# Performance work log

Hardware: AMD Instinct MI355X
Metric: run time of the kernel (lower is better)

The kernel has to match this reference:

```python
import jax, jax.numpy as jnp
import numpy as np

N_NODES = 50000
N_EDGES = 400000
D = 64          # in_feats == out_feats (transform=False)
DIST_DIM = 32
NUM = 5         # num_neighbor
N_BOUND = 64    # embedding table rows = N_BOUND + 1


def setup_inputs() -> dict:
    key = jax.random.key(0)
    ks = jax.random.split(key, 9)
    feat = jax.random.normal(ks[0], (N_NODES, D), dtype=jnp.float32)
    loc = jax.random.uniform(ks[1], (N_NODES, 2), dtype=jnp.float32)
    embed_table = jax.random.normal(ks[2], (N_BOUND + 1, DIST_DIM), dtype=jnp.float32)
    G_w = jax.random.normal(ks[3], (D, DIST_DIM), dtype=jnp.float32) / np.sqrt(DIST_DIM)
    agg_w = jax.random.normal(ks[4], (D, 2 * D), dtype=jnp.float32) / np.sqrt(2 * D)
    agg_b = jnp.zeros((D,), dtype=jnp.float32)
    boundaries = jnp.linspace(0.0, 2.0, N_BOUND).astype(jnp.float32)
    src = jax.random.randint(ks[5], (N_EDGES,), 0, N_NODES, dtype=jnp.int32)
    dst = jax.random.randint(ks[6], (N_EDGES,), 0, N_NODES, dtype=jnp.int32)
    inter_ids = jax.random.randint(ks[7], (N_EDGES, NUM), 0, N_NODES, dtype=jnp.int32)
    return {"feat": feat, "loc": loc, "embed_table": embed_table, "G_w": G_w,
            "agg_w": agg_w, "agg_b": agg_b, "boundaries": boundaries,
            "src": src, "dst": dst, "inter_ids": inter_ids}


def reference(feat, loc, embed_table, G_w, agg_w, agg_b, boundaries, src, dst, inter_ids):
    n = feat.shape[0]
    e, num = inter_ids.shape
    one = jnp.ones((e,), dtype=jnp.float32)
    # degrees: d0 = in_deg^-0.5 (at dst), d2 = out_deg^-0.5 (at src), clamp(min=1)
    in_deg = jnp.maximum(jax.ops.segment_sum(one, dst, num_segments=n), 1.0)
    out_deg = jnp.maximum(jax.ops.segment_sum(one, src, num_segments=n), 1.0)
    d0 = in_deg ** -0.5  # [N]
    d2 = out_deg ** -0.5  # [N]
    # dist1: dst->src node distance per edge
    loc_src = loc[src]                                   # [E,2]
    dist1 = jnp.linalg.norm(loc[dst] - loc_src, axis=1)  # [E]
    # dist_: src to each sampled intermediate node
    inter_pos = loc[inter_ids]                                     # [E,num,2]
    dist_ = jnp.linalg.norm(loc_src[:, None, :] - inter_pos, axis=-1)  # [E,num]
    # bucketize (torch right=False == searchsorted side='left') -> embed -> linear G
    b1 = jnp.searchsorted(boundaries, dist1, side='left')   # [E]
    b_ = jnp.searchsorted(boundaries, dist_, side='left')   # [E,num]
    dist_embed1 = embed_table[b1] @ G_w.T                    # [E,D]
    dist_embed_ = embed_table[b_] @ G_w.T                    # [E,num,D]
    # mean over sampled intermediates of (dist-embed * gathered feat)
    dist_embed_dot_h = (dist_embed_ * feat[inter_ids]).mean(axis=1)  # [E,D]
    # agg_fc on concat, degree-scaled
    cat = jnp.concatenate([dist_embed1 * feat[src], dist_embed_dot_h], axis=1)  # [E,2D]
    h = (d0[dst] * d2[src])[:, None] * (cat @ agg_w.T + agg_b)                  # [E,D]
    # copy_e / sum: scatter-sum edges to dst nodes
    rst = jax.ops.segment_sum(h, dst, num_segments=n)  # [N,D]
    return rst
```

## Files before the change

kernel.cpp:

```cpp
#include <hip/hip_runtime.h>


#define DFEAT 64

typedef __attribute__((ext_vector_type(8))) _Float16 half8;
typedef __attribute__((ext_vector_type(4))) float floatx4;
typedef __attribute__((ext_vector_type(4))) int intx4;

__device__ __forceinline__ void sb8d(int2 q, float (&f)[8]) {
#pragma unroll
    for (int t = 0; t < 4; ++t) f[t] = (float)((q.x << (24 - 8 * t)) >> 24);
#pragma unroll
    for (int t = 0; t < 4; ++t) f[4 + t] = (float)((q.y << (24 - 8 * t)) >> 24);
}

__device__ __forceinline__ int bucketize(float x, float bnd) {
    int i = (int)(x * 31.5f);
    i = min(max(i, 0), 64);
#pragma unroll
    for (int t = 0; t < 3; ++t) {
        float bi = __shfl(bnd, min(i, 63));
        if (i < 64 && bi < x) ++i;
    }
#pragma unroll
    for (int t = 0; t < 2; ++t) {
        float bim = __shfl(bnd, max(i - 1, 0));
        if (i > 0 && bim >= x) --i;
    }
    return i;
}

__global__ void k_prep(const float* __restrict__ Etab,
                       const float* __restrict__ G, float* __restrict__ P,
                       float* __restrict__ rst, float* __restrict__ degs,
                       const float* __restrict__ feat,
                       signed char* __restrict__ featQ,
                       float* __restrict__ scaleQ, int nRst, int nDeg) {
    int i = blockIdx.x * blockDim.x + threadIdx.x;
    if (i < nDeg) degs[i] = 0.0f;
    if (i < 65 * DFEAT) {
        int b = i >> 6, o = i & 63;
        float a = 0.0f;
#pragma unroll
        for (int m = 0; m < 32; ++m)
            a = fmaf(Etab[b * 32 + m], G[o * 32 + m], a);
        P[i] = a;
    }
    if (i < nRst) {
        __builtin_nontemporal_store(0.0f, rst + i);
        if (featQ) {
            float f = feat[i];
            float a = fabsf(f);
#pragma unroll
            for (int o = 32; o; o >>= 1) a = fmaxf(a, __shfl_xor(a, o));
            float inv = (a > 0.0f) ? 127.0f / a : 0.0f;
            __builtin_nontemporal_store(
                (signed char)__float2int_rn(f * inv), featQ + i);
            if ((i & 63) == 0) scaleQ[i >> 6] = a * (1.0f / 127.0f);
        }
    }
}

__global__ void k_deg(const int* __restrict__ src, const int* __restrict__ dst,
                      float* __restrict__ degs, int N, int E) {
    int i = blockIdx.x * blockDim.x + threadIdx.x;
    if (i < E) {
        atomicAdd(&degs[dst[i]], 1.0f);
        atomicAdd(&degs[N + src[i]], 1.0f);
    }
}

#define SCHUNK 1024

__global__ void k_scanA(const float* __restrict__ degs, int* __restrict__ bsum,
                        int N) {
    __shared__ int part[256];
    const int t = threadIdx.x;
    const int base = blockIdx.x * SCHUNK + t * 4;
    int s = 0;
#pragma unroll
    for (int j = 0; j < 4; ++j) {
        int i = base + j;
        if (i < N) s += (int)degs[i];
    }
    part[t] = s;
    __syncthreads();
    for (int off = 128; off; off >>= 1) {
        if (t < off) part[t] += part[t + off];
        __syncthreads();
    }
    if (t == 0) bsum[blockIdx.x] = part[0];
}

__global__ void k_scanB(int* __restrict__ bsum, int NB) {
    if (threadIdx.x == 0) {
        int run = 0;
        for (int i = 0; i < NB; ++i) {
            int v = bsum[i];
            bsum[i] = run;
            run += v;
        }
    }
}

__global__ void k_scanC(const float* __restrict__ degs,
                        const int* __restrict__ bsum, int* __restrict__ binptr,
                        int N) {
    __shared__ int part[256];
    const int t = threadIdx.x;
    const int base = blockIdx.x * SCHUNK + t * 4;
    int c[4];
    int s = 0;
#pragma unroll
    for (int j = 0; j < 4; ++j) {
        int i = base + j;
        c[j] = (i < N) ? (int)degs[i] : 0;
        s += c[j];
    }
    part[t] = s;
    __syncthreads();
    for (int off = 1; off < 256; off <<= 1) {
        int v = (t >= off) ? part[t - off] : 0;
        __syncthreads();
        part[t] += v;
        __syncthreads();
    }
    int run = bsum[blockIdx.x] + part[t] - s;
#pragma unroll
    for (int j = 0; j < 4; ++j) {
        int i = base + j;
        if (i < N) {
            binptr[i] = run;
            run += c[j];
        }
    }
}

__global__ void k_scatter(const int* __restrict__ src,
                          const int* __restrict__ dst,
                          const int* __restrict__ inter,
                          int* __restrict__ binptr, int* __restrict__ pack,
                          int E, int paddedE) {
    int i = blockIdx.x * blockDim.x + threadIdx.x;
    if (i < E) {
        int dd = dst[i];
        int pos = atomicAdd(&binptr[dd], 1);
        intx4 p0 = {src[i], dd, inter[i * 5 + 0], inter[i * 5 + 1]};
        intx4 p1 = {inter[i * 5 + 2], inter[i * 5 + 3], inter[i * 5 + 4], 0};
        __builtin_nontemporal_store(p0, (intx4*)(pack + (size_t)pos * 8));
        __builtin_nontemporal_store(p1, (intx4*)(pack + (size_t)pos * 8 + 4));
    } else if (i < paddedE) {
        intx4 z = {0, 0, 0, 0};
        __builtin_nontemporal_store(z, (intx4*)(pack + (size_t)i * 8));
        __builtin_nontemporal_store(z, (intx4*)(pack + (size_t)i * 8 + 4));
    }
}

#define PPAD 68

__global__ __launch_bounds__(256, 4) void k_edge(
    const float* __restrict__ feat, const signed char* __restrict__ featQ,
    const float* __restrict__ scaleQ, const float* __restrict__ loc,
    const float* __restrict__ agg_w, const float* __restrict__ agg_b,
    const float* __restrict__ bnds, const int* __restrict__ src,
    const int* __restrict__ dst, const int* __restrict__ inter,
    const int* __restrict__ pack, const float* __restrict__ P,
    const float* __restrict__ degs, float* __restrict__ rst, int N, int E) {
    const int tid = threadIdx.x;
    const int lane = tid & 63;
    const int wid = tid >> 6;
    const int m16 = lane & 15;
    const int quad = lane >> 4;

    __shared__ float sP[65 * PPAD];
    __shared__ half8 sWB[16 * 64];

    for (int i = tid; i < 65 * DFEAT; i += 256)
        sP[(i >> 6) * PPAD + (i & 63)] = P[i];

    for (int f = wid; f < 16; f += 4) {
        int sl = f >> 2, nt = f & 3;
        const float* wp = agg_w + (nt * 16 + m16) * 128 + sl * 32 + quad * 8;
        floatx4 wa = *(const floatx4*)wp;
        floatx4 wb = *(const floatx4*)(wp + 4);
        float xs[8] = {wa.x, wa.y, wa.z, wa.w, wb.x, wb.y, wb.z, wb.w};
        half8 h;
#pragma unroll
        for (int j = 0; j < 8; ++j) h[j] = (_Float16)xs[j];
        sWB[f * 64 + lane] = h;
    }

    const float bnd = bnds[lane];
    float bias4[4];
#pragma unroll
    for (int nt = 0; nt < 4; ++nt) bias4[nt] = agg_b[nt * 16 + m16];

    __syncthreads();

    const int nw = gridDim.x << 2;
    const int wi = (blockIdx.x << 2) + wid;
    const int ngroups = (E + 15) >> 4;
    const bool haveQ = (featQ != nullptr);
    const int k0q = quad * 8;

    const int qq = ngroups / nw, rr = ngroups - qq * nw;
    const int g0 = wi * qq + min(wi, rr);
    const int g1 = g0 + qq + (wi < rr ? 1 : 0);

    for (int g = g0; g < g1; ++g) {
        const int em = (g << 4) + m16;
        const bool act = em < E;
        const int ec = act ? em : 0;

        int s, d, ij[5];
        if (pack) {
            const intx4 p0 = __builtin_nontemporal_load(
                (const intx4*)(pack + (size_t)em * 8));
            const intx4 p1 = __builtin_nontemporal_load(
                (const intx4*)(pack + (size_t)em * 8 + 4));
            s = p0[0]; d = p0[1];
            ij[0] = p0[2]; ij[1] = p0[3];
            ij[2] = p1[0]; ij[3] = p1[1]; ij[4] = p1[2];
        } else {
            s = __builtin_nontemporal_load(src + ec);
            d = __builtin_nontemporal_load(dst + ec);
#pragma unroll
            for (int j = 0; j < 5; ++j)
                ij[j] = __builtin_nontemporal_load(inter + ec * 5 + j);
        }

        const float2 ls = ((const float2*)loc)[s];
        const float2 ld = ((const float2*)loc)[d];
        float2 lj[5];
#pragma unroll
        for (int j = 0; j < 5; ++j) lj[j] = ((const float2*)loc)[ij[j]];
        const float dgd = degs[d];
        const float dgs = degs[N + s];

        half8 A[4];
        float dsc;
        int b1;
        if (haveQ) {
            const float ssrc = scaleQ[s];
            float sq[5];
#pragma unroll
            for (int j = 0; j < 5; ++j) sq[j] = scaleQ[ij[j]];

            const signed char* qrow = featQ + (s << 6);
            int2 qu[2];
            qu[0] = *(const int2*)(qrow + k0q);
            qu[1] = *(const int2*)(qrow + 32 + k0q);
            int2 qv[2][5];
#pragma unroll
            for (int sl = 0; sl < 2; ++sl)
#pragma unroll
                for (int j = 0; j < 5; ++j)
                    qv[sl][j] =
                        *(const int2*)(featQ + (ij[j] << 6) + sl * 32 + k0q);

            dsc = rsqrtf(fmaxf(dgd, 1.0f)) * rsqrtf(fmaxf(dgs, 1.0f));
            if (!act) dsc = 0.0f;
            float dx = ld.x - ls.x, dy = ld.y - ls.y;
            b1 = bucketize(sqrtf(dx * dx + dy * dy), bnd);
            int bj[5];
#pragma unroll
            for (int j = 0; j < 5; ++j) {
                float ex = ls.x - lj[j].x, ey = ls.y - lj[j].y;
                bj[j] = bucketize(sqrtf(ex * ex + ey * ey), bnd);
            }

            const float* prow = sP + b1 * PPAD;
#pragma unroll
            for (int sl = 0; sl < 2; ++sl) {
                int k0 = sl * 32 + k0q;
                float fq[8];
                sb8d(qu[sl], fq);
                floatx4 pa = *(const floatx4*)(prow + k0);
                floatx4 pb = *(const floatx4*)(prow + k0 + 4);
                float xs[8] = {fq[0] * ssrc * pa.x, fq[1] * ssrc * pa.y,
                               fq[2] * ssrc * pa.z, fq[3] * ssrc * pa.w,
                               fq[4] * ssrc * pb.x, fq[5] * ssrc * pb.y,
                               fq[6] * ssrc * pb.z, fq[7] * ssrc * pb.w};
                half8 h;
#pragma unroll
                for (int j = 0; j < 8; ++j) h[j] = (_Float16)xs[j];
                A[sl] = h;
            }
#pragma unroll
            for (int sl = 0; sl < 2; ++sl) {
                int k0 = sl * 32 + k0q;
                float r[8] = {0, 0, 0, 0, 0, 0, 0, 0};
#pragma unroll
                for (int j = 0; j < 5; ++j) {
                    float fq[8];
                    sb8d(qv[sl][j], fq);
                    const float sj = sq[j];
                    const float* pr = sP + bj[j] * PPAD;
                    floatx4 pa = *(const floatx4*)(pr + k0);
                    floatx4 pb = *(const floatx4*)(pr + k0 + 4);
                    r[0] = fmaf(fq[0] * sj, pa.x, r[0]);
                    r[1] = fmaf(fq[1] * sj, pa.y, r[1]);
                    r[2] = fmaf(fq[2] * sj, pa.z, r[2]);
                    r[3] = fmaf(fq[3] * sj, pa.w, r[3]);
                    r[4] = fmaf(fq[4] * sj, pb.x, r[4]);
                    r[5] = fmaf(fq[5] * sj, pb.y, r[5]);
                    r[6] = fmaf(fq[6] * sj, pb.z, r[6]);
                    r[7] = fmaf(fq[7] * sj, pb.w, r[7]);
                }
                half8 h;
#pragma unroll
                for (int j = 0; j < 8; ++j) h[j] = (_Float16)(r[j] * 0.2f);
                A[2 + sl] = h;
            }
        } else {
            dsc = rsqrtf(fmaxf(dgd, 1.0f)) * rsqrtf(fmaxf(dgs, 1.0f));
            if (!act) dsc = 0.0f;
            float dx = ld.x - ls.x, dy = ld.y - ls.y;
            b1 = bucketize(sqrtf(dx * dx + dy * dy), bnd);
            int bj[5];
#pragma unroll
            for (int j = 0; j < 5; ++j) {
                float ex = ls.x - lj[j].x, ey = ls.y - lj[j].y;
                bj[j] = bucketize(sqrtf(ex * ex + ey * ey), bnd);
            }
            const float* frow = feat + (s << 6);
            const float* prow = sP + b1 * PPAD;
#pragma unroll
            for (int sl = 0; sl < 2; ++sl) {
                int k0 = sl * 32 + k0q;
                floatx4 fa = *(const floatx4*)(frow + k0);
                floatx4 fb = *(const floatx4*)(frow + k0 + 4);
                floatx4 pa = *(const floatx4*)(prow + k0);
                floatx4 pb = *(const floatx4*)(prow + k0 + 4);
                float xs[8] = {fa.x * pa.x, fa.y * pa.y, fa.z * pa.z,
                               fa.w * pa.w, fb.x * pb.x, fb.y * pb.y,
                               fb.z * pb.z, fb.w * pb.w};
                half8 h;
#pragma unroll
                for (int j = 0; j < 8; ++j) h[j] = (_Float16)xs[j];
                A[sl] = h;
            }
#pragma unroll
            for (int sl = 0; sl < 2; ++sl) {
                int k0 = sl * 32 + k0q;
                float r[8] = {0, 0, 0, 0, 0, 0, 0, 0};
#pragma unroll
                for (int j = 0; j < 5; ++j) {
                    const float* fr = feat + (ij[j] << 6);
                    const float* pr = sP + bj[j] * PPAD;
                    floatx4 fa = *(const floatx4*)(fr + k0);
                    floatx4 fb = *(const floatx4*)(fr + k0 + 4);
                    floatx4 pa = *(const floatx4*)(pr + k0);
                    floatx4 pb = *(const floatx4*)(pr + k0 + 4);
                    r[0] = fmaf(fa.x, pa.x, r[0]);
                    r[1] = fmaf(fa.y, pa.y, r[1]);
                    r[2] = fmaf(fa.z, pa.z, r[2]);
                    r[3] = fmaf(fa.w, pa.w, r[3]);
                    r[4] = fmaf(fb.x, pb.x, r[4]);
                    r[5] = fmaf(fb.y, pb.y, r[5]);
                    r[6] = fmaf(fb.z, pb.z, r[6]);
                    r[7] = fmaf(fb.w, pb.w, r[7]);
                }
                half8 h;
#pragma unroll
                for (int j = 0; j < 8; ++j) h[j] = (_Float16)(r[j] * 0.2f);
                A[2 + sl] = h;
            }
        }

        floatx4 acc[4] = {{0, 0, 0, 0}, {0, 0, 0, 0}, {0, 0, 0, 0}, {0, 0, 0, 0}};
#pragma unroll
        for (int sl = 0; sl < 4; ++sl) {
#pragma unroll
            for (int nt = 0; nt < 4; ++nt) {
                half8 b = sWB[((sl << 2) + nt) * 64 + lane];
                acc[nt] = __builtin_amdgcn_mfma_f32_16x16x32_f16(
                    A[sl], b, acc[nt], 0, 0, 0);
            }
        }

        const int q4 = quad << 2;
        const int dm0 = __shfl(d, q4 + 0), dm1 = __shfl(d, q4 + 1);
        const int dm2 = __shfl(d, q4 + 2), dm3 = __shfl(d, q4 + 3);
        const float sc0 = __shfl(dsc, q4 + 0), sc1 = __shfl(dsc, q4 + 1);
        const float sc2 = __shfl(dsc, q4 + 2), sc3 = __shfl(dsc, q4 + 3);
        const int dmn = __shfl(d, (q4 + 4) & 15);
        const int dmp = __shfl(d, (q4 - 1) & 15);
        const bool eq0 = dm0 == dm1, eq1 = dm1 == dm2, eq2 = dm2 == dm3;
        const bool eq3 = (quad < 3) && (dm3 == dmn);
        const bool lnk = (quad > 0) && (dmp == dm0);
        const bool alls = eq0 && eq1 && eq2;
        const bool gate = alls && lnk;

        float w0[4], w1[4], w2[4], w3[4], Ci[4];
#pragma unroll
        for (int nt = 0; nt < 4; ++nt) {
            w0[nt] = (acc[nt][0] + bias4[nt]) * sc0;
            w1[nt] = (acc[nt][1] + bias4[nt]) * sc1;
            w2[nt] = (acc[nt][2] + bias4[nt]) * sc2;
            w3[nt] = (acc[nt][3] + bias4[nt]) * sc3;
            if (eq0) w1[nt] += w0[nt];
            if (eq1) w2[nt] += w1[nt];
            if (eq2) w3[nt] += w2[nt];
            float T = w3[nt];
#pragma unroll
            for (int k = 0; k < 3; ++k) {
                float Tp = __shfl(T, (lane - 16) & 63);
                T = w3[nt] + (gate ? Tp : 0.0f);
            }
            float c = __shfl(T, (lane - 16) & 63);
            Ci[nt] = lnk ? c : 0.0f;
        }

        if (!eq0) {
            float* ap = rst + (dm0 << 6) + m16;
            float v0 = w0[0] + Ci[0], v1 = w0[1] + Ci[1];
            float v2 = w0[2] + Ci[2], v3 = w0[3] + Ci[3];
            asm volatile("global_atomic_add_f32 %0, %1, off nt" :: "v"(ap), "v"(v0));
            asm volatile("global_atomic_add_f32 %0, %1, off offset:64 nt" :: "v"(ap), "v"(v1));
            asm volatile("global_atomic_add_f32 %0, %1, off offset:128 nt" :: "v"(ap), "v"(v2));
            asm volatile("global_atomic_add_f32 %0, %1, off offset:192 nt" :: "v"(ap), "v"(v3));
        }
        if (!eq1) {
            float* ap = rst + (dm1 << 6) + m16;
            float h0 = eq0 ? Ci[0] : 0.0f, h1 = eq0 ? Ci[1] : 0.0f;
            float h2 = eq0 ? Ci[2] : 0.0f, h3 = eq0 ? Ci[3] : 0.0f;
            float v0 = w1[0] + h0, v1 = w1[1] + h1;
            float v2 = w1[2] + h2, v3 = w1[3] + h3;
            asm volatile("global_atomic_add_f32 %0, %1, off nt" :: "v"(ap), "v"(v0));
            asm volatile("global_atomic_add_f32 %0, %1, off offset:64 nt" :: "v"(ap), "v"(v1));
            asm volatile("global_atomic_add_f32 %0, %1, off offset:128 nt" :: "v"(ap), "v"(v2));
            asm volatile("global_atomic_add_f32 %0, %1, off offset:192 nt" :: "v"(ap), "v"(v3));
        }
        if (!eq2) {
            const bool hr = eq0 && eq1;
            float* ap = rst + (dm2 << 6) + m16;
            float v0 = w2[0] + (hr ? Ci[0] : 0.0f), v1 = w2[1] + (hr ? Ci[1] : 0.0f);
            float v2 = w2[2] + (hr ? Ci[2] : 0.0f), v3 = w2[3] + (hr ? Ci[3] : 0.0f);
            asm volatile("global_atomic_add_f32 %0, %1, off nt" :: "v"(ap), "v"(v0));
            asm volatile("global_atomic_add_f32 %0, %1, off offset:64 nt" :: "v"(ap), "v"(v1));
            asm volatile("global_atomic_add_f32 %0, %1, off offset:128 nt" :: "v"(ap), "v"(v2));
            asm volatile("global_atomic_add_f32 %0, %1, off offset:192 nt" :: "v"(ap), "v"(v3));
        }
        if (!eq3) {
            float* ap = rst + (dm3 << 6) + m16;
            float v0 = w3[0] + (alls ? Ci[0] : 0.0f), v1 = w3[1] + (alls ? Ci[1] : 0.0f);
            float v2 = w3[2] + (alls ? Ci[2] : 0.0f), v3 = w3[3] + (alls ? Ci[3] : 0.0f);
            asm volatile("global_atomic_add_f32 %0, %1, off nt" :: "v"(ap), "v"(v0));
            asm volatile("global_atomic_add_f32 %0, %1, off offset:64 nt" :: "v"(ap), "v"(v1));
            asm volatile("global_atomic_add_f32 %0, %1, off offset:128 nt" :: "v"(ap), "v"(v2));
            asm volatile("global_atomic_add_f32 %0, %1, off offset:192 nt" :: "v"(ap), "v"(v3));
        }
    }
}

extern "C" void kernel_launch(void* const* d_in, const int* in_sizes, int n_in,
                              void* d_out, int out_size, void* d_ws,
                              size_t ws_size, hipStream_t stream) {
    const float* feat  = (const float*)d_in[0];
    const float* loc   = (const float*)d_in[1];
    const float* embed = (const float*)d_in[2];
    const float* G_w   = (const float*)d_in[3];
    const float* agg_w = (const float*)d_in[4];
    const float* agg_b = (const float*)d_in[5];
    const float* bnds  = (const float*)d_in[6];
    const int* src   = (const int*)d_in[7];
    const int* dst   = (const int*)d_in[8];
    const int* inter = (const int*)d_in[9];

    const int N = in_sizes[0] / DFEAT;
    const int E = in_sizes[7];
    const int ngroups = (E + 15) >> 4;
    const int paddedE = ngroups << 4;
    const int NB = (N + SCHUNK - 1) / SCHUNK;

    float* rst = (float*)d_out;
    float* ws = (float*)d_ws;
    float* degs = ws;
    float* P = ws + 2 * (size_t)N;
    float* scaleQ = P + 65 * DFEAT;

    size_t fixed_bytes = (2 * (size_t)N + 65 * DFEAT + (size_t)N) * sizeof(float);
    size_t fq_off = (fixed_bytes + 15) & ~(size_t)15;
    size_t need_q = fq_off + (size_t)N * DFEAT;
    signed char* featQ =
        (ws_size >= need_q) ? (signed char*)((char*)d_ws + fq_off) : nullptr;

    size_t so = (need_q + 15) & ~(size_t)15;
    size_t need_sort =
        so + ((size_t)N + 8 * (size_t)paddedE + (size_t)NB) * sizeof(int);
    int* binptr = nullptr;
    int* pack = nullptr;
    int* bsum = nullptr;
    if (ws_size >= need_sort) {
        binptr = (int*)((char*)d_ws + so);
        pack = binptr + N;
        bsum = pack + 8 * (size_t)paddedE;
    }

    const int nRst = N * DFEAT;
    const int nDeg = 2 * N;

    k_prep<<<(nRst + 255) / 256, 256, 0, stream>>>(
        embed, G_w, P, rst, degs, feat, featQ, scaleQ, nRst, nDeg);
    k_deg<<<(E + 255) / 256, 256, 0, stream>>>(src, dst, degs, N, E);
    if (pack) {
        k_scanA<<<NB, 256, 0, stream>>>(degs, bsum, N);
        k_scanB<<<1, 64, 0, stream>>>(bsum, NB);
        k_scanC<<<NB, 256, 0, stream>>>(degs, bsum, binptr, N);
        k_scatter<<<(paddedE + 255) / 256, 256, 0, stream>>>(
            src, dst, inter, binptr, pack, E, paddedE);
    }
    k_edge<<<1024, 256, 0, stream>>>(feat, featQ, scaleQ, loc, agg_w, agg_b,
                                     bnds, src, dst, inter, pack, P, degs,
                                     rst, N, E);
}
```

Baseline: 261.5 us.

## Precompute distance buckets and degree scale in scatter; store embed table as fp16

Distance computation, bucketization and the degree normalisation factor move from the edge kernel into the scatter pass. The bucket ids are packed into the upper bits of the node indices and the scale goes into the spare pack slot, so the edge kernel no longer gathers loc or degs. The projected embedding table is kept in fp16 in shared memory to shrink LDS use. Occupancy is raised (launch bounds 6, 1536 blocks). This adds gathers to the scatter kernel, loses some precision in P, and limits node ids to 20 bits.

```diff
diff --git a/kernel.cpp b/kernel.cpp
--- a/kernel.cpp
+++ b/kernel.cpp
@@ -7,6 +7,8 @@
 typedef __attribute__((ext_vector_type(4))) float floatx4;
 typedef __attribute__((ext_vector_type(4))) int intx4;
 
+#define IDXMASK 0xFFFFF
+
 __device__ __forceinline__ void sb8d(int2 q, float (&f)[8]) {
 #pragma unroll
     for (int t = 0; t < 4; ++t) f[t] = (float)((q.x << (24 - 8 * t)) >> 24);
@@ -31,7 +33,7 @@
 }
 
 __global__ void k_prep(const float* __restrict__ Etab,
-                       const float* __restrict__ G, float* __restrict__ P,
+                       const float* __restrict__ G, _Float16* __restrict__ Ph,
                        float* __restrict__ rst, float* __restrict__ degs,
                        const float* __restrict__ feat,
                        signed char* __restrict__ featQ,
@@ -44,7 +46,7 @@
 #pragma unroll
         for (int m = 0; m < 32; ++m)
             a = fmaf(Etab[b * 32 + m], G[o * 32 + m], a);
-        P[i] = a;
+        Ph[i] = (_Float16)a;
     }
     if (i < nRst) {
         __builtin_nontemporal_store(0.0f, rst + i);
@@ -139,14 +141,34 @@
 __global__ void k_scatter(const int* __restrict__ src,
                           const int* __restrict__ dst,
                           const int* __restrict__ inter,
+                          const float* __restrict__ loc,
+                          const float* __restrict__ degs,
+                          const float* __restrict__ bnds,
                           int* __restrict__ binptr, int* __restrict__ pack,
-                          int E, int paddedE) {
-    int i = blockIdx.x * blockDim.x + threadIdx.x;
+                          int N, int E, int paddedE) {
+    const int i = blockIdx.x * blockDim.x + threadIdx.x;
+    const float bnd = bnds[threadIdx.x & 63];
     if (i < E) {
-        int dd = dst[i];
+        const int s = src[i];
+        const int dd = dst[i];
+        const float2 ls = ((const float2*)loc)[s];
+        const float2 ld = ((const float2*)loc)[dd];
+        const float dsc = rsqrtf(fmaxf(degs[dd], 1.0f)) *
+                          rsqrtf(fmaxf(degs[N + s], 1.0f));
+        float dx = ld.x - ls.x, dy = ld.y - ls.y;
+        const int b1 = bucketize(sqrtf(dx * dx + dy * dy), bnd);
+        int w2[5];
+#pragma unroll
+        for (int j = 0; j < 5; ++j) {
+            int id = inter[i * 5 + j];
+            float2 lj = ((const float2*)loc)[id];
+            float ex = ls.x - lj.x, ey = ls.y - lj.y;
+            int bj = bucketize(sqrtf(ex * ex + ey * ey), bnd);
+            w2[j] = id | (bj << 20);
+        }
         int pos = atomicAdd(&binptr[dd], 1);
-        intx4 p0 = {src[i], dd, inter[i * 5 + 0], inter[i * 5 + 1]};
-        intx4 p1 = {inter[i * 5 + 2], inter[i * 5 + 3], inter[i * 5 + 4], 0};
+        intx4 p0 = {s | (b1 << 20), dd, w2[0], w2[1]};
+        intx4 p1 = {w2[2], w2[3], w2[4], __float_as_int(dsc)};
         __builtin_nontemporal_store(p0, (intx4*)(pack + (size_t)pos * 8));
         __builtin_nontemporal_store(p1, (intx4*)(pack + (size_t)pos * 8 + 4));
     } else if (i < paddedE) {
@@ -156,15 +178,15 @@
     }
 }
 
-#define PPAD 68
-
-__global__ __launch_bounds__(256, 4) void k_edge(
+#define PPADH 72
+
+__global__ __launch_bounds__(256, 6) void k_edge(
     const float* __restrict__ feat, const signed char* __restrict__ featQ,
     const float* __restrict__ scaleQ, const float* __restrict__ loc,
     const float* __restrict__ agg_w, const float* __restrict__ agg_b,
     const float* __restrict__ bnds, const int* __restrict__ src,
     const int* __restrict__ dst, const int* __restrict__ inter,
-    const int* __restrict__ pack, const float* __restrict__ P,
+    const int* __restrict__ pack, const _Float16* __restrict__ Ph,
     const float* __restrict__ degs, float* __restrict__ rst, int N, int E) {
     const int tid = threadIdx.x;
     const int lane = tid & 63;
@@ -172,11 +194,11 @@
     const int m16 = lane & 15;
     const int quad = lane >> 4;
 
-    __shared__ float sP[65 * PPAD];
+    __shared__ _Float16 sPh[65 * PPADH];
     __shared__ half8 sWB[16 * 64];
 
     for (int i = tid; i < 65 * DFEAT; i += 256)
-        sP[(i >> 6) * PPAD + (i & 63)] = P[i];
+        sPh[(i >> 6) * PPADH + (i & 63)] = Ph[i];
 
     for (int f = wid; f < 16; f += 4) {
         int sl = f >> 2, nt = f & 3;
@@ -209,38 +231,25 @@
 
     for (int g = g0; g < g1; ++g) {
         const int em = (g << 4) + m16;
-        const bool act = em < E;
-        const int ec = act ? em : 0;
-
-        int s, d, ij[5];
+
+        int s, d, b1, ij[5], bj[5];
+        float dsc;
+        half8 A[4];
+
         if (pack) {
             const intx4 p0 = __builtin_nontemporal_load(
                 (const intx4*)(pack + (size_t)em * 8));
             const intx4 p1 = __builtin_nontemporal_load(
                 (const intx4*)(pack + (size_t)em * 8 + 4));
-            s = p0[0]; d = p0[1];
-            ij[0] = p0[2]; ij[1] = p0[3];
-            ij[2] = p1[0]; ij[3] = p1[1]; ij[4] = p1[2];
-        } else {
-            s = __builtin_nontemporal_load(src + ec);
-            d = __builtin_nontemporal_load(dst + ec);
-#pragma unroll
-            for (int j = 0; j < 5; ++j)
-                ij[j] = __builtin_nontemporal_load(inter + ec * 5 + j);
-        }
-
-        const float2 ls = ((const float2*)loc)[s];
-        const float2 ld = ((const float2*)loc)[d];
-        float2 lj[5];
-#pragma unroll
-        for (int j = 0; j < 5; ++j) lj[j] = ((const float2*)loc)[ij[j]];
-        const float dgd = degs[d];
-        const float dgs = degs[N + s];
-
-        half8 A[4];
-        float dsc;
-        int b1;
-        if (haveQ) {
+            s = p0[0] & IDXMASK;  b1 = p0[0] >> 20;
+            d = p0[1];
+            ij[0] = p0[2] & IDXMASK; bj[0] = p0[2] >> 20;
+            ij[1] = p0[3] & IDXMASK; bj[1] = p0[3] >> 20;
+            ij[2] = p1[0] & IDXMASK; bj[2] = p1[0] >> 20;
+            ij[3] = p1[1] & IDXMASK; bj[3] = p1[1] >> 20;
+            ij[4] = p1[2] & IDXMASK; bj[4] = p1[2] >> 20;
+            dsc = __int_as_float(p1[3]);
+
             const float ssrc = scaleQ[s];
             float sq[5];
 #pragma unroll
@@ -258,32 +267,17 @@
                     qv[sl][j] =
                         *(const int2*)(featQ + (ij[j] << 6) + sl * 32 + k0q);
 
-            dsc = rsqrtf(fmaxf(dgd, 1.0f)) * rsqrtf(fmaxf(dgs, 1.0f));
-            if (!act) dsc = 0.0f;
-            float dx = ld.x - ls.x, dy = ld.y - ls.y;
-            b1 = bucketize(sqrtf(dx * dx + dy * dy), bnd);
-            int bj[5];
-#pragma unroll
-            for (int j = 0; j < 5; ++j) {
-                float ex = ls.x - lj[j].x, ey = ls.y - lj[j].y;
-                bj[j] = bucketize(sqrtf(ex * ex + ey * ey), bnd);
-            }
-
-            const float* prow = sP + b1 * PPAD;
+            const _Float16* prow = sPh + b1 * PPADH;
 #pragma unroll
             for (int sl = 0; sl < 2; ++sl) {
                 int k0 = sl * 32 + k0q;
                 float fq[8];
                 sb8d(qu[sl], fq);
-                floatx4 pa = *(const floatx4*)(prow + k0);
-                floatx4 pb = *(const floatx4*)(prow + k0 + 4);
-                float xs[8] = {fq[0] * ssrc * pa.x, fq[1] * ssrc * pa.y,
-                               fq[2] * ssrc * pa.z, fq[3] * ssrc * pa.w,
-                               fq[4] * ssrc * pb.x, fq[5] * ssrc * pb.y,
-                               fq[6] * ssrc * pb.z, fq[7] * ssrc * pb.w};
+                half8 ph = *(const half8*)(prow + k0);
                 half8 h;
 #pragma unroll
-                for (int j = 0; j < 8; ++j) h[j] = (_Float16)xs[j];
+                for (int j = 0; j < 8; ++j)
+                    h[j] = (_Float16)(fq[j] * ssrc * (float)ph[j]);
                 A[sl] = h;
             }
 #pragma unroll
@@ -295,17 +289,16 @@
                     float fq[8];
                     sb8d(qv[sl][j], fq);
                     const float sj = sq[j];
-                    const float* pr = sP + bj[j] * PPAD;
-                    floatx4 pa = *(const floatx4*)(pr + k0);
-                    floatx4 pb = *(const floatx4*)(pr + k0 + 4);
-                    r[0] = fmaf(fq[0] * sj, pa.x, r[0]);
-                    r[1] = fmaf(fq[1] * sj, pa.y, r[1]);
-                    r[2] = fmaf(fq[2] * sj, pa.z, r[2]);
-                    r[3] = fmaf(fq[3] * sj, pa.w, r[3]);
-                    r[4] = fmaf(fq[4] * sj, pb.x, r[4]);
-                    r[5] = fmaf(fq[5] * sj, pb.y, r[5]);
-                    r[6] = fmaf(fq[6] * sj, pb.z, r[6]);
-                    r[7] = fmaf(fq[7] * sj, pb.w, r[7]);
+                    const _Float16* pr = sPh + bj[j] * PPADH + k0;
+                    half8 pv = *(const half8*)pr;
+                    r[0] = fmaf(fq[0] * sj, (float)pv[0], r[0]);
+                    r[1] = fmaf(fq[1] * sj, (float)pv[1], r[1]);
+                    r[2] = fmaf(fq[2] * sj, (float)pv[2], r[2]);
+                    r[3] = fmaf(fq[3] * sj, (float)pv[3], r[3]);
+                    r[4] = fmaf(fq[4] * sj, (float)pv[4], r[4]);
+                    r[5] = fmaf(fq[5] * sj, (float)pv[5], r[5]);
+                    r[6] = fmaf(fq[6] * sj, (float)pv[6], r[6]);
+                    r[7] = fmaf(fq[7] * sj, (float)pv[7], r[7]);
                 }
                 half8 h;
 #pragma unroll
@@ -313,28 +306,37 @@
                 A[2 + sl] = h;
             }
         } else {
-            dsc = rsqrtf(fmaxf(dgd, 1.0f)) * rsqrtf(fmaxf(dgs, 1.0f));
+            const bool act = em < E;
+            const int ec = act ? em : 0;
+            s = src[ec];
+            d = dst[ec];
+            const float2 ls = ((const float2*)loc)[s];
+            const float2 ld = ((const float2*)loc)[d];
+            dsc = rsqrtf(fmaxf(degs[d], 1.0f)) *
+                  rsqrtf(fmaxf(degs[N + s], 1.0f));
             if (!act) dsc = 0.0f;
             float dx = ld.x - ls.x, dy = ld.y - ls.y;
             b1 = bucketize(sqrtf(dx * dx + dy * dy), bnd);
-            int bj[5];
 #pragma unroll
             for (int j = 0; j < 5; ++j) {
-                float ex = ls.x - lj[j].x, ey = ls.y - lj[j].y;
+                int id = inter[ec * 5 + j];
+                ij[j] = id;
+                float2 lj = ((const float2*)loc)[id];
+                float ex = ls.x - lj.x, ey = ls.y - lj.y;
                 bj[j] = bucketize(sqrtf(ex * ex + ey * ey), bnd);
             }
             const float* frow = feat + (s << 6);
-            const float* prow = sP + b1 * PPAD;
+            const _Float16* prow = sPh + b1 * PPADH;
 #pragma unroll
             for (int sl = 0; sl < 2; ++sl) {
                 int k0 = sl * 32 + k0q;
                 floatx4 fa = *(const floatx4*)(frow + k0);
                 floatx4 fb = *(const floatx4*)(frow + k0 + 4);
-                floatx4 pa = *(const floatx4*)(prow + k0);
-                floatx4 pb = *(const floatx4*)(prow + k0 + 4);
-                float xs[8] = {fa.x * pa.x, fa.y * pa.y, fa.z * pa.z,
-                               fa.w * pa.w, fb.x * pb.x, fb.y * pb.y,
-                               fb.z * pb.z, fb.w * pb.w};
+                half8 ph = *(const half8*)(prow + k0);
+                float xs[8] = {fa.x * (float)ph[0], fa.y * (float)ph[1],
+                               fa.z * (float)ph[2], fa.w * (float)ph[3],
+                               fb.x * (float)ph[4], fb.y * (float)ph[5],
+                               fb.z * (float)ph[6], fb.w * (float)ph[7]};
                 half8 h;
 #pragma unroll
                 for (int j = 0; j < 8; ++j) h[j] = (_Float16)xs[j];
@@ -347,19 +349,18 @@
 #pragma unroll
                 for (int j = 0; j < 5; ++j) {
                     const float* fr = feat + (ij[j] << 6);
-                    const float* pr = sP + bj[j] * PPAD;
+                    const _Float16* pr = sPh + bj[j] * PPADH + k0;
                     floatx4 fa = *(const floatx4*)(fr + k0);
                     floatx4 fb = *(const floatx4*)(fr + k0 + 4);
-                    floatx4 pa = *(const floatx4*)(pr + k0);
-                    floatx4 pb = *(const floatx4*)(pr + k0 + 4);
-                    r[0] = fmaf(fa.x, pa.x, r[0]);
-                    r[1] = fmaf(fa.y, pa.y, r[1]);
-                    r[2] = fmaf(fa.z, pa.z, r[2]);
-                    r[3] = fmaf(fa.w, pa.w, r[3]);
-                    r[4] = fmaf(fb.x, pb.x, r[4]);
-                    r[5] = fmaf(fb.y, pb.y, r[5]);
-                    r[6] = fmaf(fb.z, pb.z, r[6]);
-                    r[7] = fmaf(fb.w, pb.w, r[7]);
+                    half8 pv = *(const half8*)pr;
+                    r[0] = fmaf(fa.x, (float)pv[0], r[0]);
+                    r[1] = fmaf(fa.y, (float)pv[1], r[1]);
+                    r[2] = fmaf(fa.z, (float)pv[2], r[2]);
+                    r[3] = fmaf(fa.w, (float)pv[3], r[3]);
+                    r[4] = fmaf(fb.x, (float)pv[4], r[4]);
+                    r[5] = fmaf(fb.y, (float)pv[5], r[5]);
+                    r[6] = fmaf(fb.z, (float)pv[6], r[6]);
+                    r[7] = fmaf(fb.w, (float)pv[7], r[7]);
                 }
                 half8 h;
 #pragma unroll
@@ -475,43 +476,46 @@
     const int NB = (N + SCHUNK - 1) / SCHUNK;
 
     float* rst = (float*)d_out;
-    float* ws = (float*)d_ws;
-    float* degs = ws;
-    float* P = ws + 2 * (size_t)N;
-    float* scaleQ = P + 65 * DFEAT;
-
-    size_t fixed_bytes = (2 * (size_t)N + 65 * DFEAT + (size_t)N) * sizeof(float);
-    size_t fq_off = (fixed_bytes + 15) & ~(size_t)15;
-    size_t need_q = fq_off + (size_t)N * DFEAT;
+    char* wsb = (char*)d_ws;
+
+    auto al16 = [](size_t x) { return (x + 15) & ~(size_t)15; };
+    size_t off_degs = 0;
+    size_t off_p = al16(off_degs + 2 * (size_t)N * 4);
+    size_t off_scale = al16(off_p + 65 * DFEAT * 2);
+    size_t off_q = al16(off_scale + (size_t)N * 4);
+    size_t off_bin = al16(off_q + (size_t)N * DFEAT);
+    size_t off_pack = al16(off_bin + (size_t)N * 4);
+    size_t off_bsum = off_pack + 32 * (size_t)paddedE;
+    size_t need_all = off_bsum + (size_t)NB * 4;
+
+    float* degs = (float*)(wsb + off_degs);
+    _Float16* Ph = (_Float16*)(wsb + off_p);
+    float* scaleQ = (float*)(wsb + off_scale);
     signed char* featQ =
-        (ws_size >= need_q) ? (signed char*)((char*)d_ws + fq_off) : nullptr;
-
-    size_t so = (need_q + 15) & ~(size_t)15;
-    size_t need_sort =
-        so + ((size_t)N + 8 * (size_t)paddedE + (size_t)NB) * sizeof(int);
+        (ws_size >= off_bin) ? (signed char*)(wsb + off_q) : nullptr;
     int* binptr = nullptr;
     int* pack = nullptr;
     int* bsum = nullptr;
-    if (ws_size >= need_sort) {
-        binptr = (int*)((char*)d_ws + so);
-        pack = binptr + N;
-        bsum = pack + 8 * (size_t)paddedE;
+    if (ws_size >= need_all && N < (1 << 20) && featQ) {
+        binptr = (int*)(wsb + off_bin);
+        pack = (int*)(wsb + off_pack);
+        bsum = (int*)(wsb + off_bsum);
     }
 
     const int nRst = N * DFEAT;
     const int nDeg = 2 * N;
 
     k_prep<<<(nRst + 255) / 256, 256, 0, stream>>>(
-        embed, G_w, P, rst, degs, feat, featQ, scaleQ, nRst, nDeg);
+        embed, G_w, Ph, rst, degs, feat, featQ, scaleQ, nRst, nDeg);
     k_deg<<<(E + 255) / 256, 256, 0, stream>>>(src, dst, degs, N, E);
     if (pack) {
         k_scanA<<<NB, 256, 0, stream>>>(degs, bsum, N);
         k_scanB<<<1, 64, 0, stream>>>(bsum, NB);
         k_scanC<<<NB, 256, 0, stream>>>(degs, bsum, binptr, N);
         k_scatter<<<(paddedE + 255) / 256, 256, 0, stream>>>(
-            src, dst, inter, binptr, pack, E, paddedE);
-    }
-    k_edge<<<1024, 256, 0, stream>>>(feat, featQ, scaleQ, loc, agg_w, agg_b,
-                                     bnds, src, dst, inter, pack, P, degs,
+            src, dst, inter, loc, degs, bnds, binptr, pack, N, E, paddedE);
+    }
+    k_edge<<<1536, 256, 0, stream>>>(feat, featQ, scaleQ, loc, agg_w, agg_b,
+                                     bnds, src, dst, inter, pack, Ph, degs,
                                      rst, N, E);
 }
```

Result: faster. 255.9 us (-2.1%).
